# Kernel optimization log

Hardware: AMD Instinct MI355X
Metric: run time of the kernel (lower is better)

The kernel has to match this reference:

```python
import jax, jax.numpy as jnp
import numpy as np

WS = 8   # window size
NH = 8   # num heads


def layernorm(x, g, b, eps=1e-5):
    m = jnp.mean(x, axis=-1, keepdims=True)
    v = jnp.var(x, axis=-1, keepdims=True)
    return (x - m) * jax.lax.rsqrt(v + eps) * g + b


def setup_inputs() -> dict:
    key = jax.random.key(0)
    ks = jax.random.split(key, 8)
    B, C, H, W = 16, 256, 64, 64
    s = 0.02
    inp = {
        "x": jax.random.normal(ks[0], (B, C, H, W), jnp.float32),
        "norm1_g": jnp.ones((C,), jnp.float32),
        "norm1_b": jnp.zeros((C,), jnp.float32),
        "qkv_w": jax.random.normal(ks[1], (3 * C, C), jnp.float32) * s,
        "qkv_b": jnp.zeros((3 * C,), jnp.float32),
        "rel_bias_table": jax.random.normal(ks[2], ((2 * WS - 1) ** 2, NH), jnp.float32) * s,
        "proj_w": jax.random.normal(ks[3], (C, C), jnp.float32) * s,
        "proj_b": jnp.zeros((C,), jnp.float32),
        "norm2_g": jnp.ones((C,), jnp.float32),
        "norm2_b": jnp.zeros((C,), jnp.float32),
        "fc1_w": jax.random.normal(ks[4], (4 * C, C), jnp.float32) * s,
        "fc1_b": jnp.zeros((4 * C,), jnp.float32),
        "fc2_w": jax.random.normal(ks[5], (C, 4 * C), jnp.float32) * s,
        "fc2_b": jnp.zeros((C,), jnp.float32),
    }
    # relative position index (Swin standard), shape (WS*WS, WS*WS), int constant
    coords = np.stack(np.meshgrid(np.arange(WS), np.arange(WS), indexing="ij")).reshape(2, -1)
    rel = (coords[:, :, None] - coords[:, None, :]).transpose(1, 2, 0)
    rel[:, :, 0] += WS - 1
    rel[:, :, 1] += WS - 1
    rel[:, :, 0] *= 2 * WS - 1
    inp["rel_index"] = jnp.asarray(rel.sum(-1), jnp.int32)
    return inp


def reference(x, norm1_g, norm1_b, qkv_w, qkv_b, rel_bias_table, proj_w, proj_b,
              norm2_g, norm2_b, fc1_w, fc1_b, fc2_w, fc2_b, rel_index):
    B, C, H, W = x.shape
    N = WS * WS
    hd = C // NH
    scale = hd ** -0.5

    xs = jnp.transpose(x, (0, 2, 3, 1)).reshape(B, H * W, C)  # b (h w) c
    shortcut = xs

    y = layernorm(xs, norm1_g, norm1_b).reshape(B, H, W, C)
    # window partition -> (B*nW, N, C); shift_size = 0 (default), no cyclic shift / mask
    y = y.reshape(B, H // WS, WS, W // WS, WS, C).transpose(0, 1, 3, 2, 4, 5).reshape(-1, N, C)

    qkv = (y @ qkv_w.T + qkv_b).reshape(-1, N, 3, NH, hd).transpose(2, 0, 3, 1, 4)
    q, k, v = qkv[0], qkv[1], qkv[2]  # each (nW*B, NH, N, hd)

    attn = jnp.einsum("whnd,whmd->whnm", q * scale, k)
    bias = rel_bias_table[rel_index].transpose(2, 0, 1)  # (NH, N, N)
    attn = jax.nn.softmax(attn + bias[None], axis=-1)
    out = jnp.einsum("whnm,whmd->whnd", attn, v).transpose(0, 2, 1, 3).reshape(-1, N, C)
    out = out @ proj_w.T + proj_b

    # window reverse -> (B, H*W, C)
    out = out.reshape(B, H // WS, W // WS, WS, WS, C).transpose(0, 1, 3, 2, 4, 5).reshape(B, H * W, C)

    xs = shortcut + out
    h = layernorm(xs, norm2_g, norm2_b)
    h = jax.nn.gelu(h @ fc1_w.T + fc1_b, approximate=False) @ fc2_w.T + fc2_b
    xs = xs + h

    return jnp.transpose(xs.reshape(B, H, W, C), (0, 3, 1, 2))
```

## Files before the change

### kernel.cpp

```cpp
#include <hip/hip_runtime.h>

typedef unsigned short u16;
typedef __attribute__((ext_vector_type(8))) short short8;
typedef __attribute__((ext_vector_type(4))) float f32x4;
typedef __attribute__((ext_vector_type(16))) float f32x16;

#define MFMA32(a, b, c) __builtin_amdgcn_mfma_f32_32x32x16_bf16((a), (b), (c), 0, 0, 0)
#define MFMA16(a, b, c) __builtin_amdgcn_mfma_f32_16x16x32_bf16((a), (b), (c), 0, 0, 0)
#define WAITV(N) asm volatile("s_waitcnt vmcnt(" #N ")" ::: "memory")
#define BARS() __builtin_amdgcn_s_barrier()
#define MFENCE() asm volatile("" ::: "memory")

__device__ __forceinline__ u16 f2b(float f) {
  unsigned b = __float_as_uint(f);
  b += 0x7FFFu + ((b >> 16) & 1u);
  return (u16)(b >> 16);
}
__device__ __forceinline__ float b2f(u16 u) { return __uint_as_float(((unsigned)u) << 16); }

__device__ __forceinline__ unsigned cvt2(float lo, float hi) {
  unsigned r;
  asm("v_cvt_pk_bf16_f32 %0, %1, %2" : "=v"(r) : "v"(lo), "v"(hi));
  return r;
}

__device__ __forceinline__ void gload_lds16(const void* g, void* l) {
  __builtin_amdgcn_global_load_lds((const __attribute__((address_space(1))) void*)g,
                                   (__attribute__((address_space(3))) void*)l, 16, 0, 0);
}

__device__ __forceinline__ float fast_gelu(float x) {
  const float x2 = x * x;
  const float z = x * (1.5957691216f + 0.0713548162f * x2);
  const float e = __expf(-z);
  float r;
  asm("v_rcp_f32 %0, %1" : "=v"(r) : "v"(1.f + e));
  return x * r;
}

__global__ __launch_bounds__(256) void prep_kernel(
    const float* __restrict__ qkv_w, const float* __restrict__ proj_w,
    const float* __restrict__ fc1_w, const float* __restrict__ fc2_w,
    const float* __restrict__ tbl, const int* __restrict__ ridx,
    u16* __restrict__ wqkv, u16* __restrict__ wproj, u16* __restrict__ wfc1,
    u16* __restrict__ wfc2, float* __restrict__ bfull) {
  int i = blockIdx.x * 256 + threadIdx.x;
  if (i < 196608) {
    wqkv[i] = f2b(qkv_w[i]);
  } else if (i < 262144) {
    wproj[i - 196608] = f2b(proj_w[i - 196608]);
  } else if (i < 524288) {
    wfc1[i - 262144] = f2b(fc1_w[i - 262144]);
  } else if (i < 786432) {
    wfc2[i - 524288] = f2b(fc2_w[i - 524288]);
  } else {
    int j = i - 786432;
    int hm = j >> 12, nm = j & 4095;
    bfull[j] = tbl[ridx[nm] * 8 + hm];
  }
}

__global__ __launch_bounds__(256) void ln1_win_kernel(const float* __restrict__ x,
                                                      const float* __restrict__ g,
                                                      const float* __restrict__ b,
                                                      u16* __restrict__ y,
                                                      u16* __restrict__ xsb) {
  __shared__ float red[2][4][64];
  const int bh = blockIdx.x;
  const int bb = bh >> 6, h = bh & 63;
  const int w = threadIdx.x & 63, cg = threadIdx.x >> 6;
  const float* xp = x + (size_t)bb * 1048576 + (size_t)h * 64 + w;
  float vals[64];
  float s = 0.f, ss = 0.f;
#pragma unroll
  for (int j = 0; j < 64; ++j) {
    float v = xp[(size_t)(cg * 64 + j) * 4096];
    vals[j] = v;
    s += v;
    ss += v * v;
  }
  red[0][cg][w] = s;
  red[1][cg][w] = ss;
  __syncthreads();
  const float S = red[0][0][w] + red[0][1][w] + red[0][2][w] + red[0][3][w];
  const float Q = red[1][0][w] + red[1][1][w] + red[1][2][w] + red[1][3][w];
  const float m = S * (1.f / 256.f);
  const float rstd = rsqrtf(Q * (1.f / 256.f) - m * m + 1e-5f);
  const int win = bb * 64 + ((h >> 3) << 3) + (w >> 3);
  const int tok = ((h & 7) << 3) + (w & 7);
  const size_t base = (size_t)win * 16384 + tok * 256 + cg * 64;
#pragma unroll
  for (int jj = 0; jj < 8; ++jj) {
    short8 o, raw;
#pragma unroll
    for (int q = 0; q < 8; ++q) {
      const int c64 = jj * 8 + q;
      const int c = cg * 64 + c64;
      raw[q] = (short)f2b(vals[c64]);
      o[q] = (short)f2b((vals[c64] - m) * rstd * g[c] + b[c]);
    }
    *(short8*)&y[base + jj * 8] = o;
    *(short8*)&xsb[base + jj * 8] = raw;
  }
}

template <int EPI, int KT, int NNT>
__global__ __launch_bounds__(256, 6) void gemm_bt(const u16* __restrict__ A,
                                                  const u16* __restrict__ W,
                                                  const float* __restrict__ bias,
                                                  u16* __restrict__ outh,
                                                  float* __restrict__ outf,
                                                  const u16* __restrict__ aux) {
  constexpr int NTK = KT >> 5;
  constexpr int NC = NNT * 128;
  __shared__ __align__(16) u16 As[2][4096];
  __shared__ __align__(16) u16 Bs[2][4096];
  const int xcd = blockIdx.x & 7, ii = blockIdx.x >> 3;
  const int mt = xcd * 64 + ii / NNT;
  const int nt = ii % NNT;
  const int tid = threadIdx.x;
  const int wv = tid >> 6, lane = tid & 63;
  const int wr = (wv >> 1) << 6;
  const int wc = (wv & 1) << 6;
  const int srow = tid >> 2;
  const int sslot = (((tid & 3) ^ ((tid >> 5) & 3)) << 3);
  const int l31 = lane & 31, lh = lane >> 5;
  const int xk = (l31 >> 3) & 3;
  f32x16 acc[2][2];
#pragma unroll
  for (int ti = 0; ti < 2; ++ti)
#pragma unroll
    for (int tj = 0; tj < 2; ++tj)
#pragma unroll
      for (int e = 0; e < 16; ++e) acc[ti][tj][e] = 0.f;
  const u16* Ab = A + (size_t)mt * 128 * KT;
  const u16* Wb = W + (size_t)nt * 128 * KT;

#define STG(BF, T)                                                                      \
  {                                                                                     \
    const int kt_ = (T) << 5;                                                           \
    gload_lds16(Ab + (size_t)srow * KT + kt_ + sslot, &As[BF][tid * 8]);                \
    gload_lds16(Ab + (size_t)(srow + 64) * KT + kt_ + sslot, &As[BF][2048 + tid * 8]);  \
    gload_lds16(Wb + (size_t)srow * KT + kt_ + sslot, &Bs[BF][tid * 8]);                \
    gload_lds16(Wb + (size_t)(srow + 64) * KT + kt_ + sslot, &Bs[BF][2048 + tid * 8]);  \
  }
#define CMPT(BF)                                                                        \
  {                                                                                     \
    short8 a_[2][2], b_[2][2];                                                          \
    _Pragma("unroll") for (int ti = 0; ti < 2; ++ti)                                    \
        _Pragma("unroll") for (int kk = 0; kk < 2; ++kk)                                \
            a_[ti][kk] = *(const short8*)&As[BF][(wr + ti * 32 + l31) * 32 +            \
                                                (((kk * 2 + lh) ^ xk) << 3)];           \
    _Pragma("unroll") for (int tj = 0; tj < 2; ++tj)                                    \
        _Pragma("unroll") for (int kk = 0; kk < 2; ++kk)                                \
            b_[tj][kk] = *(const short8*)&Bs[BF][(wc + tj * 32 + l31) * 32 +            \
                                                (((kk * 2 + lh) ^ xk) << 3)];           \
    _Pragma("unroll") for (int kk = 0; kk < 2; ++kk)                                    \
        _Pragma("unroll") for (int ti = 0; ti < 2; ++ti)                                \
            _Pragma("unroll") for (int tj = 0; tj < 2; ++tj)                            \
                acc[ti][tj] = MFMA32(a_[ti][kk], b_[tj][kk], acc[ti][tj]);              \
  }

  STG(0, 0);
  STG(1, 1);
  int rr = 0;
  for (int t = 0; t < NTK; ++t) {
    if (t + 1 < NTK) {
      WAITV(4);
    } else {
      WAITV(0);
    }
    BARS();
    MFENCE();
    CMPT(rr);
    MFENCE();
    BARS();
    if (t + 2 < NTK) STG(rr, t + 2);
    rr ^= 1;
  }
#undef STG
#undef CMPT

  const int row0 = mt * 128 + wr + lh * 4;
  const int colL = nt * 128 + wc + l31;

  if constexpr (EPI == 0) {
#pragma unroll
    for (int ti = 0; ti < 2; ++ti)
#pragma unroll
      for (int tj = 0; tj < 2; ++tj) {
        const int col = colL + tj * 32;
        const int which = col >> 8, cc = col & 255;
        u16* dst = outh + (size_t)which * 16777216ull;
        const float scl = (which == 0) ? 0.17677669529663689f : 1.0f;
        const float bv = bias[col];
#pragma unroll
        for (int rg = 0; rg < 4; ++rg) {
          const int rowb = row0 + ti * 32 + rg * 8;
          const unsigned p01 = cvt2((acc[ti][tj][rg * 4 + 0] + bv) * scl,
                                    (acc[ti][tj][rg * 4 + 1] + bv) * scl);
          const unsigned p23 = cvt2((acc[ti][tj][rg * 4 + 2] + bv) * scl,
                                    (acc[ti][tj][rg * 4 + 3] + bv) * scl);
          dst[(size_t)(rowb + 0) * 256 + cc] = (u16)p01;
          dst[(size_t)(rowb + 1) * 256 + cc] = (u16)(p01 >> 16);
          dst[(size_t)(rowb + 2) * 256 + cc] = (u16)p23;
          dst[(size_t)(rowb + 3) * 256 + cc] = (u16)(p23 >> 16);
        }
      }
  } else if constexpr (EPI == 2) {
#pragma unroll
    for (int ti = 0; ti < 2; ++ti)
#pragma unroll
      for (int tj = 0; tj < 2; ++tj) {
        const int col = colL + tj * 32;
        const float bv = bias[col];
#pragma unroll
        for (int rg = 0; rg < 4; ++rg) {
          const int rowb = row0 + ti * 32 + rg * 8;
          const unsigned p01 = cvt2(fast_gelu(acc[ti][tj][rg * 4 + 0] + bv),
                                    fast_gelu(acc[ti][tj][rg * 4 + 1] + bv));
          const unsigned p23 = cvt2(fast_gelu(acc[ti][tj][rg * 4 + 2] + bv),
                                    fast_gelu(acc[ti][tj][rg * 4 + 3] + bv));
          outh[(size_t)(rowb + 0) * NC + col] = (u16)p01;
          outh[(size_t)(rowb + 1) * NC + col] = (u16)(p01 >> 16);
          outh[(size_t)(rowb + 2) * NC + col] = (u16)p23;
          outh[(size_t)(rowb + 3) * NC + col] = (u16)(p23 >> 16);
        }
      }
  } else {
#pragma unroll
    for (int ti = 0; ti < 2; ++ti)
#pragma unroll
      for (int tj = 0; tj < 2; ++tj) {
        const int col = colL + tj * 32;
        const float bv = bias[col];
#pragma unroll
        for (int rg = 0; rg < 4; ++rg) {
          const int rowb = row0 + ti * 32 + rg * 8;
          const int win = rowb >> 6, tk = rowb & 63;
          const int bb = win >> 6;
          const int h = (((win >> 3) & 7) << 3) + (tk >> 3);
          const int w = ((win & 7) << 3) + (tk & 7);
          f32x4 v;
#pragma unroll
          for (int rq = 0; rq < 4; ++rq)
            v[rq] = acc[ti][tj][rg * 4 + rq] + bv + b2f(aux[(size_t)(rowb + rq) * 256 + col]);
          *(f32x4*)&outf[(((size_t)bb * 256 + col) * 64 + h) * 64 + w] = v;
        }
      }
  }
}

__global__ __launch_bounds__(512) void proj_ln2(const u16* __restrict__ A,
                                                const u16* __restrict__ W,
                                                const float* __restrict__ bias,
                                                const u16* __restrict__ xsb,
                                                const float* __restrict__ g2,
                                                const float* __restrict__ b2,
                                                u16* __restrict__ xs2b,
                                                u16* __restrict__ h2) {
  __shared__ __align__(16) u16 As[2][4096];
  __shared__ __align__(16) u16 Bs[2][8192];
  __shared__ float redS[4][128], redQ[4][128];
  const int mt = blockIdx.x;
  const int tid = threadIdx.x;
  const int wv = tid >> 6, lane = tid & 63;
  const int wm = wv >> 2, wn = wv & 3;
  const int rowa = tid >> 2;
  const int esl = (((tid & 3) ^ ((tid >> 3) & 3)) << 3);
  const int lr = lane & 15, lg = lane >> 4;
  const int kq = ((lg ^ ((lr >> 1) & 3)) << 3);
  f32x4 acc[4][4];
#pragma unroll
  for (int mi = 0; mi < 4; ++mi)
#pragma unroll
    for (int ni = 0; ni < 4; ++ni) acc[mi][ni] = (f32x4){0.f, 0.f, 0.f, 0.f};
  const u16* Ab = A + (size_t)mt * 128 * 256;

#define STG(BF, T)                                                                      \
  {                                                                                     \
    const int kt_ = (T) << 5;                                                           \
    gload_lds16(Ab + (size_t)rowa * 256 + kt_ + esl, &As[BF][tid * 8]);                 \
    gload_lds16(W + (size_t)rowa * 256 + kt_ + esl, &Bs[BF][tid * 8]);                  \
    gload_lds16(W + (size_t)(rowa + 128) * 256 + kt_ + esl, &Bs[BF][tid * 8 + 4096]);   \
  }
#define CMPT(BF)                                                                        \
  {                                                                                     \
    short8 a_[4], b_[4];                                                                \
    _Pragma("unroll") for (int mi = 0; mi < 4; ++mi)                                    \
        a_[mi] = *(const short8*)&As[BF][(wm * 64 + mi * 16 + lr) * 32 + kq];           \
    _Pragma("unroll") for (int ni = 0; ni < 4; ++ni)                                    \
        b_[ni] = *(const short8*)&Bs[BF][(wn * 64 + ni * 16 + lr) * 32 + kq];           \
    _Pragma("unroll") for (int mi = 0; mi < 4; ++mi)                                    \
        _Pragma("unroll") for (int ni = 0; ni < 4; ++ni)                                \
            acc[mi][ni] = MFMA16(a_[mi], b_[ni], acc[mi][ni]);                          \
  }

  STG(0, 0);
  STG(1, 1);
  int rr = 0;
  for (int t = 0; t < 8; ++t) {
    if (t + 1 < 8) {
      WAITV(3);
    } else {
      WAITV(0);
    }
    BARS();
    MFENCE();
    CMPT(rr);
    MFENCE();
    BARS();
    if (t + 2 < 8) STG(rr, t + 2);
    rr ^= 1;
  }
#undef STG
#undef CMPT

  const int row0 = mt * 128 + wm * 64 + lg * 4;
  const int col0 = wn * 64 + lr;

#pragma unroll
  for (int mi = 0; mi < 4; ++mi)
#pragma unroll
    for (int ni = 0; ni < 4; ++ni) {
      const int col = col0 + ni * 16;
      const float bv = bias[col];
#pragma unroll
      for (int r = 0; r < 4; ++r)
        acc[mi][ni][r] += bv + b2f(xsb[(size_t)(row0 + mi * 16 + r) * 256 + col]);
    }
#pragma unroll
  for (int mi = 0; mi < 4; ++mi)
#pragma unroll
    for (int r = 0; r < 4; ++r) {
      float s = acc[mi][0][r] + acc[mi][1][r] + acc[mi][2][r] + acc[mi][3][r];
      float q = acc[mi][0][r] * acc[mi][0][r] + acc[mi][1][r] * acc[mi][1][r] +
                acc[mi][2][r] * acc[mi][2][r] + acc[mi][3][r] * acc[mi][3][r];
      s += __shfl_xor(s, 1); q += __shfl_xor(q, 1);
      s += __shfl_xor(s, 2); q += __shfl_xor(q, 2);
      s += __shfl_xor(s, 4); q += __shfl_xor(q, 4);
      s += __shfl_xor(s, 8); q += __shfl_xor(q, 8);
      if (lr == 0) {
        const int rl = wm * 64 + mi * 16 + lg * 4 + r;
        redS[wn][rl] = s;
        redQ[wn][rl] = q;
      }
    }
  __syncthreads();
#pragma unroll
  for (int mi = 0; mi < 4; ++mi)
#pragma unroll
    for (int r = 0; r < 4; ++r) {
      const int rl = wm * 64 + mi * 16 + lg * 4 + r;
      const float S = redS[0][rl] + redS[1][rl] + redS[2][rl] + redS[3][rl];
      const float Q = redQ[0][rl] + redQ[1][rl] + redQ[2][rl] + redQ[3][rl];
      const float m = S * (1.f / 256.f);
      const float rstd = rsqrtf(Q * (1.f / 256.f) - m * m + 1e-5f);
      const size_t row = row0 + mi * 16 + r;
#pragma unroll
      for (int ni = 0; ni < 4; ++ni) {
        const int col = col0 + ni * 16;
        const float v = acc[mi][ni][r];
        xs2b[row * 256 + col] = f2b(v);
        h2[row * 256 + col] = f2b((v - m) * rstd * g2[col] + b2[col]);
      }
    }
}

__global__ __launch_bounds__(64) void attn_kernel(const u16* __restrict__ qkv,
                                                  const float* __restrict__ biasf,
                                                  u16* __restrict__ aout) {
  __shared__ __align__(16) u16 sqk[5120];
  __shared__ __align__(16) u16 vt[2304];
  u16* qs = sqk;
  u16* ks = sqk + 2560;
  u16* pp = sqk;
  const int wh = blockIdx.x;
  const int head = wh & 7;
  const int win = wh >> 3;
  const int lane = threadIdx.x;
  const int lr = lane & 15, lg = lane >> 4;
  const size_t rbase = (size_t)win * 16384 + head * 32;
  const u16* qg = qkv + rbase;
  const u16* kg = qkv + 16777216ull + rbase;
  const u16* vg = qkv + 33554432ull + rbase;
#pragma unroll
  for (int i = 0; i < 4; ++i) {
    int ch = i * 64 + lane;
    int r = ch >> 2, qo = (ch & 3) * 8;
    *(short8*)&qs[r * 40 + qo] = *(const short8*)&qg[(size_t)r * 256 + qo];
    *(short8*)&ks[r * 40 + qo] = *(const short8*)&kg[(size_t)r * 256 + qo];
  }
  {
    short8 v0 = *(const short8*)&vg[(size_t)lane * 256];
    short8 v1 = *(const short8*)&vg[(size_t)lane * 256 + 8];
    short8 v2 = *(const short8*)&vg[(size_t)lane * 256 + 16];
    short8 v3 = *(const short8*)&vg[(size_t)lane * 256 + 24];
#pragma unroll
    for (int j = 0; j < 8; ++j) {
      vt[j * 72 + lane] = (u16)v0[j];
      vt[(8 + j) * 72 + lane] = (u16)v1[j];
      vt[(16 + j) * 72 + lane] = (u16)v2[j];
      vt[(24 + j) * 72 + lane] = (u16)v3[j];
    }
  }
  __syncthreads();
  f32x4 sf[4][4];
#pragma unroll
  for (int mi = 0; mi < 4; ++mi)
#pragma unroll
    for (int ni = 0; ni < 4; ++ni) sf[mi][ni] = (f32x4){0.f, 0.f, 0.f, 0.f};
  {
    short8 a[4], bq[4];
#pragma unroll
    for (int mi = 0; mi < 4; ++mi) a[mi] = *(const short8*)&qs[(mi * 16 + lr) * 40 + lg * 8];
#pragma unroll
    for (int ni = 0; ni < 4; ++ni) bq[ni] = *(const short8*)&ks[(ni * 16 + lr) * 40 + lg * 8];
#pragma unroll
    for (int mi = 0; mi < 4; ++mi)
#pragma unroll
      for (int ni = 0; ni < 4; ++ni) sf[mi][ni] = MFMA16(a[mi], bq[ni], sf[mi][ni]);
  }
  __syncthreads();
  const float* bh = biasf + (size_t)head * 4096;
#pragma unroll
  for (int mi = 0; mi < 4; ++mi) {
#pragma unroll
    for (int r = 0; r < 4; ++r) {
      const int n = mi * 16 + lg * 4 + r;
      float v0 = sf[mi][0][r] + bh[n * 64 + lr];
      float v1 = sf[mi][1][r] + bh[n * 64 + 16 + lr];
      float v2 = sf[mi][2][r] + bh[n * 64 + 32 + lr];
      float v3 = sf[mi][3][r] + bh[n * 64 + 48 + lr];
      float mx = fmaxf(fmaxf(v0, v1), fmaxf(v2, v3));
      mx = fmaxf(mx, __shfl_xor(mx, 1));
      mx = fmaxf(mx, __shfl_xor(mx, 2));
      mx = fmaxf(mx, __shfl_xor(mx, 4));
      mx = fmaxf(mx, __shfl_xor(mx, 8));
      float e0 = __expf(v0 - mx), e1 = __expf(v1 - mx);
      float e2 = __expf(v2 - mx), e3 = __expf(v3 - mx);
      float sm = e0 + e1 + e2 + e3;
      sm += __shfl_xor(sm, 1);
      sm += __shfl_xor(sm, 2);
      sm += __shfl_xor(sm, 4);
      sm += __shfl_xor(sm, 8);
      const float inv = 1.f / sm;
      pp[n * 72 + lr] = f2b(e0 * inv);
      pp[n * 72 + 16 + lr] = f2b(e1 * inv);
      pp[n * 72 + 32 + lr] = f2b(e2 * inv);
      pp[n * 72 + 48 + lr] = f2b(e3 * inv);
    }
  }
  __syncthreads();
  f32x4 o[4][2];
#pragma unroll
  for (int mi = 0; mi < 4; ++mi)
#pragma unroll
    for (int ni = 0; ni < 2; ++ni) o[mi][ni] = (f32x4){0.f, 0.f, 0.f, 0.f};
#pragma unroll
  for (int kk = 0; kk < 2; ++kk) {
    short8 pa[4], vb[2];
#pragma unroll
    for (int mi = 0; mi < 4; ++mi)
      pa[mi] = *(const short8*)&pp[(mi * 16 + lr) * 72 + kk * 32 + lg * 8];
#pragma unroll
    for (int ni = 0; ni < 2; ++ni)
      vb[ni] = *(const short8*)&vt[(ni * 16 + lr) * 72 + kk * 32 + lg * 8];
#pragma unroll
    for (int mi = 0; mi < 4; ++mi)
#pragma unroll
      for (int ni = 0; ni < 2; ++ni) o[mi][ni] = MFMA16(pa[mi], vb[ni], o[mi][ni]);
  }
  u16* op = aout + (size_t)win * 16384 + head * 32;
#pragma unroll
  for (int mi = 0; mi < 4; ++mi)
#pragma unroll
    for (int ni = 0; ni < 2; ++ni)
#pragma unroll
      for (int r = 0; r < 4; ++r) {
        const int n = mi * 16 + lg * 4 + r;
        op[(size_t)n * 256 + ni * 16 + lr] = f2b(o[mi][ni][r]);
      }
}

extern "C" void kernel_launch(void* const* d_in, const int* in_sizes, int n_in,
                              void* d_out, int out_size, void* d_ws, size_t ws_size,
                              hipStream_t stream) {
  const float* x = (const float*)d_in[0];
  const float* n1g = (const float*)d_in[1];
  const float* n1b = (const float*)d_in[2];
  const float* qkv_w = (const float*)d_in[3];
  const float* qkv_b = (const float*)d_in[4];
  const float* tbl = (const float*)d_in[5];
  const float* proj_w = (const float*)d_in[6];
  const float* proj_b = (const float*)d_in[7];
  const float* n2g = (const float*)d_in[8];
  const float* n2b = (const float*)d_in[9];
  const float* fc1_w = (const float*)d_in[10];
  const float* fc1_b = (const float*)d_in[11];
  const float* fc2_w = (const float*)d_in[12];
  const float* fc2_b = (const float*)d_in[13];
  const int* relidx = (const int*)d_in[14];
  float* outp = (float*)d_out;

  char* w = (char*)d_ws;
  const size_t Mi = 1ull << 20;
  if (ws_size < 237 * Mi) return;
  u16* Y = (u16*)(w + 0);
  u16* qb = (u16*)(w + 32 * Mi);
  u16* aout = (u16*)(w + 0);
  u16* xs2b = (u16*)(w + 0);
  u16* h2 = (u16*)(w + 32 * Mi);
  u16* xsb = (u16*)(w + 128 * Mi);
  u16* h1 = (u16*)(w + 64 * Mi);
  u16* wqkv = (u16*)(w + 192 * Mi);
  u16* wproj = wqkv + 196608;
  u16* wfc1 = wproj + 65536;
  u16* wfc2 = wfc1 + 262144;
  float* bfull = (float*)(w + 192 * Mi + 1572864);

  prep_kernel<<<3200, 256, 0, stream>>>(qkv_w, proj_w, fc1_w, fc2_w, tbl, relidx, wqkv,
                                        wproj, wfc1, wfc2, bfull);
  ln1_win_kernel<<<1024, 256, 0, stream>>>(x, n1g, n1b, Y, xsb);
  gemm_bt<0, 256, 6><<<3072, 256, 0, stream>>>(Y, wqkv, qkv_b, qb, nullptr, nullptr);
  attn_kernel<<<8192, 64, 0, stream>>>(qb, bfull, aout);
  proj_ln2<<<512, 512, 0, stream>>>(aout, wproj, proj_b, xsb, n2g, n2b, xs2b, h2);
  gemm_bt<2, 256, 8><<<4096, 256, 0, stream>>>(h2, wfc1, fc1_b, h1, nullptr, nullptr);
  gemm_bt<3, 1024, 2><<<1024, 256, 0, stream>>>(h1, wfc2, fc2_b, nullptr, outp, xs2b);
}
```

Measured before the change: 300.9 us.

## Make GEMM blocks process several M tiles with prefetch across tile boundaries

Each GEMM block now loops over CHUNK consecutive M tiles instead of one. The global-to-LDS prefetch continues into the next tile's K-slices while the current tile's epilogue runs, and the grid shrinks to match. The aim is to amortize block launch and pipeline fill/drain costs and to overlap epilogue stores with loads. The trade-off is fewer blocks, which may leave CUs underfilled on wide hardware, plus a large vmcnt wait whose correctness rests on outstanding epilogue store counts.

Result: slower. 517.0 us (+71.8%).

```diff
diff --git a/kernel.cpp b/kernel.cpp
--- a/kernel.cpp
+++ b/kernel.cpp
@@ -104,7 +104,7 @@
   }
 }
 
-template <int EPI, int KT, int NNT>
+template <int EPI, int KT, int NNT, int CHUNK>
 __global__ __launch_bounds__(256, 6) void gemm_bt(const u16* __restrict__ A,
                                                   const u16* __restrict__ W,
                                                   const float* __restrict__ bias,
@@ -112,12 +112,15 @@
                                                   float* __restrict__ outf,
                                                   const u16* __restrict__ aux) {
   constexpr int NTK = KT >> 5;
+  constexpr int NPH = NTK * CHUNK;
+  constexpr int GRP = 64 / CHUNK;
   constexpr int NC = NNT * 128;
   __shared__ __align__(16) u16 As[2][4096];
   __shared__ __align__(16) u16 Bs[2][4096];
   const int xcd = blockIdx.x & 7, ii = blockIdx.x >> 3;
-  const int mt = xcd * 64 + ii / NNT;
+  const int mtg = xcd * GRP + ii / NNT;
   const int nt = ii % NNT;
+  const int mt0 = mtg * CHUNK;
   const int tid = threadIdx.x;
   const int wv = tid >> 6, lane = tid & 63;
   const int wr = (wv >> 1) << 6;
@@ -133,14 +136,14 @@
     for (int tj = 0; tj < 2; ++tj)
 #pragma unroll
       for (int e = 0; e < 16; ++e) acc[ti][tj][e] = 0.f;
-  const u16* Ab = A + (size_t)mt * 128 * KT;
   const u16* Wb = W + (size_t)nt * 128 * KT;
 
 #define STG(BF, T)                                                                      \
   {                                                                                     \
-    const int kt_ = (T) << 5;                                                           \
-    gload_lds16(Ab + (size_t)srow * KT + kt_ + sslot, &As[BF][tid * 8]);                \
-    gload_lds16(Ab + (size_t)(srow + 64) * KT + kt_ + sslot, &As[BF][2048 + tid * 8]);  \
+    const u16* Ab_ = A + (size_t)(mt0 + (T) / NTK) * 128 * KT;                          \
+    const int kt_ = ((T) % NTK) << 5;                                                   \
+    gload_lds16(Ab_ + (size_t)srow * KT + kt_ + sslot, &As[BF][tid * 8]);               \
+    gload_lds16(Ab_ + (size_t)(srow + 64) * KT + kt_ + sslot, &As[BF][2048 + tid * 8]); \
     gload_lds16(Wb + (size_t)srow * KT + kt_ + sslot, &Bs[BF][tid * 8]);                \
     gload_lds16(Wb + (size_t)(srow + 64) * KT + kt_ + sslot, &Bs[BF][2048 + tid * 8]);  \
   }
@@ -161,94 +164,109 @@
                 acc[ti][tj] = MFMA32(a_[ti][kk], b_[tj][kk], acc[ti][tj]);              \
   }
 
+  const int colL = nt * 128 + wc + l31;
+
+  auto epilog = [&](int mtcur) {
+    const int row0 = mtcur * 128 + wr + lh * 4;
+    if constexpr (EPI == 0) {
+#pragma unroll
+      for (int ti = 0; ti < 2; ++ti)
+#pragma unroll
+        for (int tj = 0; tj < 2; ++tj) {
+          const int col = colL + tj * 32;
+          const int which = col >> 8, cc = col & 255;
+          u16* dst = outh + (size_t)which * 16777216ull;
+          const float scl = (which == 0) ? 0.17677669529663689f : 1.0f;
+          const float bv = bias[col];
+#pragma unroll
+          for (int rg = 0; rg < 4; ++rg) {
+            const int rowb = row0 + ti * 32 + rg * 8;
+            const unsigned p01 = cvt2((acc[ti][tj][rg * 4 + 0] + bv) * scl,
+                                      (acc[ti][tj][rg * 4 + 1] + bv) * scl);
+            const unsigned p23 = cvt2((acc[ti][tj][rg * 4 + 2] + bv) * scl,
+                                      (acc[ti][tj][rg * 4 + 3] + bv) * scl);
+            dst[(size_t)(rowb + 0) * 256 + cc] = (u16)p01;
+            dst[(size_t)(rowb + 1) * 256 + cc] = (u16)(p01 >> 16);
+            dst[(size_t)(rowb + 2) * 256 + cc] = (u16)p23;
+            dst[(size_t)(rowb + 3) * 256 + cc] = (u16)(p23 >> 16);
+          }
+        }
+    } else if constexpr (EPI == 2) {
+#pragma unroll
+      for (int ti = 0; ti < 2; ++ti)
+#pragma unroll
+        for (int tj = 0; tj < 2; ++tj) {
+          const int col = colL + tj * 32;
+          const float bv = bias[col];
+#pragma unroll
+          for (int rg = 0; rg < 4; ++rg) {
+            const int rowb = row0 + ti * 32 + rg * 8;
+            const unsigned p01 = cvt2(fast_gelu(acc[ti][tj][rg * 4 + 0] + bv),
+                                      fast_gelu(acc[ti][tj][rg * 4 + 1] + bv));
+            const unsigned p23 = cvt2(fast_gelu(acc[ti][tj][rg * 4 + 2] + bv),
+                                      fast_gelu(acc[ti][tj][rg * 4 + 3] + bv));
+            outh[(size_t)(rowb + 0) * NC + col] = (u16)p01;
+            outh[(size_t)(rowb + 1) * NC + col] = (u16)(p01 >> 16);
+            outh[(size_t)(rowb + 2) * NC + col] = (u16)p23;
+            outh[(size_t)(rowb + 3) * NC + col] = (u16)(p23 >> 16);
+          }
+        }
+    } else {
+#pragma unroll
+      for (int ti = 0; ti < 2; ++ti)
+#pragma unroll
+        for (int tj = 0; tj < 2; ++tj) {
+          const int col = colL + tj * 32;
+          const float bv = bias[col];
+#pragma unroll
+          for (int rg = 0; rg < 4; ++rg) {
+            const int rowb = row0 + ti * 32 + rg * 8;
+            const int win = rowb >> 6, tk = rowb & 63;
+            const int bb = win >> 6;
+            const int h = (((win >> 3) & 7) << 3) + (tk >> 3);
+            const int w = ((win & 7) << 3) + (tk & 7);
+            f32x4 v;
+#pragma unroll
+            for (int rq = 0; rq < 4; ++rq)
+              v[rq] =
+                  acc[ti][tj][rg * 4 + rq] + bv + b2f(aux[(size_t)(rowb + rq) * 256 + col]);
+            *(f32x4*)&outf[(((size_t)bb * 256 + col) * 64 + h) * 64 + w] = v;
+          }
+        }
+    }
+#pragma unroll
+    for (int ti = 0; ti < 2; ++ti)
+#pragma unroll
+      for (int tj = 0; tj < 2; ++tj)
+#pragma unroll
+        for (int e = 0; e < 16; ++e) acc[ti][tj][e] = 0.f;
+  };
+
   STG(0, 0);
   STG(1, 1);
-  int rr = 0;
-  for (int t = 0; t < NTK; ++t) {
-    if (t + 1 < NTK) {
-      WAITV(4);
-    } else {
-      WAITV(0);
-    }
-    BARS();
-    MFENCE();
-    CMPT(rr);
-    MFENCE();
-    BARS();
-    if (t + 2 < NTK) STG(rr, t + 2);
-    rr ^= 1;
+#pragma unroll
+  for (int m = 0; m < CHUNK; ++m) {
+#pragma unroll
+    for (int p = 0; p < NTK; ++p) {
+      const int g = m * NTK + p;
+      if (g == NPH - 1) {
+        WAITV(0);
+      } else if (m > 0 && p < 2) {
+        WAITV(48);
+      } else {
+        WAITV(4);
+      }
+      BARS();
+      MFENCE();
+      CMPT(g & 1);
+      MFENCE();
+      BARS();
+      if (g + 2 < NPH) STG(g & 1, g + 2);
+    }
+    epilog(mt0 + m);
   }
 #undef STG
 #undef CMPT
-
-  const int row0 = mt * 128 + wr + lh * 4;
-  const int colL = nt * 128 + wc + l31;
-
-  if constexpr (EPI == 0) {
-#pragma unroll
-    for (int ti = 0; ti < 2; ++ti)
-#pragma unroll
-      for (int tj = 0; tj < 2; ++tj) {
-        const int col = colL + tj * 32;
-        const int which = col >> 8, cc = col & 255;
-        u16* dst = outh + (size_t)which * 16777216ull;
-        const float scl = (which == 0) ? 0.17677669529663689f : 1.0f;
-        const float bv = bias[col];
-#pragma unroll
-        for (int rg = 0; rg < 4; ++rg) {
-          const int rowb = row0 + ti * 32 + rg * 8;
-          const unsigned p01 = cvt2((acc[ti][tj][rg * 4 + 0] + bv) * scl,
-                                    (acc[ti][tj][rg * 4 + 1] + bv) * scl);
-          const unsigned p23 = cvt2((acc[ti][tj][rg * 4 + 2] + bv) * scl,
-                                    (acc[ti][tj][rg * 4 + 3] + bv) * scl);
-          dst[(size_t)(rowb + 0) * 256 + cc] = (u16)p01;
-          dst[(size_t)(rowb + 1) * 256 + cc] = (u16)(p01 >> 16);
-          dst[(size_t)(rowb + 2) * 256 + cc] = (u16)p23;
-          dst[(size_t)(rowb + 3) * 256 + cc] = (u16)(p23 >> 16);
-        }
-      }
-  } else if constexpr (EPI == 2) {
-#pragma unroll
-    for (int ti = 0; ti < 2; ++ti)
-#pragma unroll
-      for (int tj = 0; tj < 2; ++tj) {
-        const int col = colL + tj * 32;
-        const float bv = bias[col];
-#pragma unroll
-        for (int rg = 0; rg < 4; ++rg) {
-          const int rowb = row0 + ti * 32 + rg * 8;
-          const unsigned p01 = cvt2(fast_gelu(acc[ti][tj][rg * 4 + 0] + bv),
-                                    fast_gelu(acc[ti][tj][rg * 4 + 1] + bv));
-          const unsigned p23 = cvt2(fast_gelu(acc[ti][tj][rg * 4 + 2] + bv),
-                                    fast_gelu(acc[ti][tj][rg * 4 + 3] + bv));
-          outh[(size_t)(rowb + 0) * NC + col] = (u16)p01;
-          outh[(size_t)(rowb + 1) * NC + col] = (u16)(p01 >> 16);
-          outh[(size_t)(rowb + 2) * NC + col] = (u16)p23;
-          outh[(size_t)(rowb + 3) * NC + col] = (u16)(p23 >> 16);
-        }
-      }
-  } else {
-#pragma unroll
-    for (int ti = 0; ti < 2; ++ti)
-#pragma unroll
-      for (int tj = 0; tj < 2; ++tj) {
-        const int col = colL + tj * 32;
-        const float bv = bias[col];
-#pragma unroll
-        for (int rg = 0; rg < 4; ++rg) {
-          const int rowb = row0 + ti * 32 + rg * 8;
-          const int win = rowb >> 6, tk = rowb & 63;
-          const int bb = win >> 6;
-          const int h = (((win >> 3) & 7) << 3) + (tk >> 3);
-          const int w = ((win & 7) << 3) + (tk & 7);
-          f32x4 v;
-#pragma unroll
-          for (int rq = 0; rq < 4; ++rq)
-            v[rq] = acc[ti][tj][rg * 4 + rq] + bv + b2f(aux[(size_t)(rowb + rq) * 256 + col]);
-          *(f32x4*)&outf[(((size_t)bb * 256 + col) * 64 + h) * 64 + w] = v;
-        }
-      }
-  }
 }
 
 __global__ __launch_bounds__(512) void proj_ln2(const u16* __restrict__ A,
@@ -522,9 +540,9 @@
   prep_kernel<<<3200, 256, 0, stream>>>(qkv_w, proj_w, fc1_w, fc2_w, tbl, relidx, wqkv,
                                         wproj, wfc1, wfc2, bfull);
   ln1_win_kernel<<<1024, 256, 0, stream>>>(x, n1g, n1b, Y, xsb);
-  gemm_bt<0, 256, 6><<<3072, 256, 0, stream>>>(Y, wqkv, qkv_b, qb, nullptr, nullptr);
+  gemm_bt<0, 256, 6, 4><<<768, 256, 0, stream>>>(Y, wqkv, qkv_b, qb, nullptr, nullptr);
   attn_kernel<<<8192, 64, 0, stream>>>(qb, bfull, aout);
   proj_ln2<<<512, 512, 0, stream>>>(aout, wproj, proj_b, xsb, n2g, n2b, xs2b, h2);
-  gemm_bt<2, 256, 8><<<4096, 256, 0, stream>>>(h2, wfc1, fc1_b, h1, nullptr, nullptr);
-  gemm_bt<3, 1024, 2><<<1024, 256, 0, stream>>>(h1, wfc2, fc2_b, nullptr, outp, xs2b);
-}
+  gemm_bt<2, 256, 8, 4><<<1024, 256, 0, stream>>>(h2, wfc1, fc1_b, h1, nullptr, nullptr);
+  gemm_bt<3, 1024, 2, 2><<<512, 256, 0, stream>>>(h1, wfc2, fc2_b, nullptr, outp, xs2b);
+}
```
